# Kernel optimization log

Hardware: AMD Instinct MI355X
Metric: run time of the kernel (lower is better)

Reference implementation:

```python
import jax, jax.numpy as jnp
import numpy as np

B, NC, CN, K, DN = 2, 256, 256, 16, 64
G, HM, HS, HMOD, MOD_OUT = 8, 128, 128, 64, 5


def setup_inputs() -> dict:
    rng = np.random.default_rng(0)
    # per-neuron top-K neighbors within cell, excluding self, sorted (matches torch buffer build)
    scores = rng.random((NC, CN, CN)).astype(np.float32)
    ii = np.arange(CN)
    scores[:, ii, ii] = -np.inf
    conn = np.argpartition(-scores, K, axis=-1)[..., :K]
    conn = np.sort(conn, axis=-1).astype(np.int32)  # [NC, CN, K]

    key = jax.random.key(0)
    ks = jax.random.split(key, 12)
    n = lambda k, s, sc=1.0: jax.random.normal(k, s, jnp.float32) * sc
    return {
        'h': n(ks[0], (B, NC, CN, DN), 0.01),
        'w_conn': n(ks[1], (B, NC, CN, K), 0.1),
        'cell_context': n(ks[2], (B, NC, DN), 0.1),
        'neuron_id': n(ks[3], (NC, CN, DN), 0.02),
        'msg_w1': n(ks[4], (G, HM, 3 * DN), 0.05), 'msg_b1': jnp.zeros((G, HM)),
        'msg_w2': n(ks[5], (G, DN, HM), 0.005), 'msg_b2': jnp.zeros((G, DN)),
        'state_w1': n(ks[6], (G, HS, 3 * DN), 0.05), 'state_b1': jnp.zeros((G, HS)),
        'state_w2': n(ks[7], (G, DN, HS), 0.005), 'state_b2': jnp.zeros((G, DN)),
        'mod_w1': n(ks[8], (NC, 2 * DN, HMOD), 0.05), 'mod_b1': jnp.zeros((NC, HMOD)),
        'mod_w2': n(ks[9], (NC, HMOD, MOD_OUT), 0.0005), 'mod_b2': jnp.zeros((NC, MOD_OUT)),
        'conn_idx': jnp.asarray(conn),
        'cell_to_group': (jnp.arange(NC) % G).astype(jnp.int32),
    }


def reference(h, w_conn, cell_context, neuron_id,
              msg_w1, msg_b1, msg_w2, msg_b2,
              state_w1, state_b1, state_w2, state_b2,
              mod_w1, mod_b1, mod_w2, mod_b2,
              conn_idx, cell_to_group):
    nc = h.shape[1]
    cell_ix = jnp.arange(nc)[:, None, None]
    # gather K-neighbor states per neuron: [B, NC, CN, K, DN]
    nb = jax.vmap(lambda hb: hb[cell_ix, conn_idx])(h)
    # connection-weighted aggregation
    agg = jnp.einsum('bnck,bnckd->bncd', w_conn, nb)

    g = cell_to_group  # [NC]
    # grouped message MLP (2-layer), per-cell weights gathered from group table
    mfeat = jnp.concatenate([h, agg, jnp.broadcast_to(neuron_id[None], h.shape)], axis=-1)
    mh = jax.nn.gelu(jnp.einsum('bncf,nhf->bnch', mfeat, msg_w1[g]) + msg_b1[g][None, :, None, :])
    msg = jnp.einsum('bnch,ndh->bncd', mh, msg_w2[g]) + msg_b2[g][None, :, None, :]

    # grouped state MLP, residual update on h
    ctx = jnp.broadcast_to(cell_context[:, :, None, :], h.shape)
    sfeat = jnp.concatenate([h, msg, ctx], axis=-1)
    sh = jax.nn.gelu(jnp.einsum('bncf,nhf->bnch', sfeat, state_w1[g]) + state_b1[g][None, :, None, :])
    h_new = h + jnp.einsum('bnch,ndh->bncd', sh, state_w2[g]) + state_b2[g][None, :, None, :]

    # per-cell modulation MLP on pooled stats (h_mean || msg_mean)
    pooled = jnp.concatenate([h_new.mean(axis=2), msg.mean(axis=2)], axis=-1)  # [B, NC, 2DN]
    ph = jax.nn.gelu(jnp.einsum('bnf,nfh->bnh', pooled, mod_w1) + mod_b1[None])
    mod = jnp.einsum('bnh,nho->bno', ph, mod_w2) + mod_b2[None]
    return h_new, msg, mod
```

## Files before the change

### kernel.cpp

```cpp
#include <hip/hip_runtime.h>

#define B_   2
#define NC_  256
#define CN_  256
#define K_   16
#define DN_  64
#define G_   8
#define HM_  128
#define F3_  192

typedef unsigned short u16;
typedef short v8s __attribute__((ext_vector_type(8)));
typedef float v4f __attribute__((ext_vector_type(4)));

#define SMEM_BYTES 63616


__device__ __forceinline__ u16 f2b(float f) {
    unsigned v; __builtin_memcpy(&v, &f, 4);
    v = v + 0x7fffu + ((v >> 16) & 1u);
    return (u16)(v >> 16);
}
__device__ __forceinline__ v8s cvt8(const float* p) {
    float4 a = *(const float4*)p, b = *(const float4*)(p + 4);
    v8s r;
    r[0] = (short)f2b(a.x); r[1] = (short)f2b(a.y); r[2] = (short)f2b(a.z); r[3] = (short)f2b(a.w);
    r[4] = (short)f2b(b.x); r[5] = (short)f2b(b.y); r[6] = (short)f2b(b.z); r[7] = (short)f2b(b.w);
    return r;
}
__device__ __forceinline__ float gelu_t(float x) {
    float u = x * x;
    float t = 1.5957691216057308f * x * __builtin_fmaf(0.044715f, u, 1.0f);
    float e = __expf(-t);
    return x * __builtin_amdgcn_rcpf(1.0f + e);
}

__global__ __launch_bounds__(256) void cvt_w(
    const float* __restrict__ mw1, const float* __restrict__ mw2,
    const float* __restrict__ sw1, const float* __restrict__ sw2,
    u16* __restrict__ dst)
{
    int e = (blockIdx.x * 256 + threadIdx.x) * 4;
    const float* s; int off;
    if      (e < 196608) { s = mw1; off = e; }
    else if (e < 262144) { s = mw2; off = e - 196608; }
    else if (e < 458752) { s = sw1; off = e - 262144; }
    else                 { s = sw2; off = e - 458752; }
    float4 v = *(const float4*)(s + off);
    ushort4 o4;
    o4.x = f2b(v.x); o4.y = f2b(v.y); o4.z = f2b(v.z); o4.w = f2b(v.w);
    *(ushort4*)(dst + e) = o4;
}

__global__ __launch_bounds__(256, 2) void mg_main(
    const float* __restrict__ h,    const float* __restrict__ wconn,
    const float* __restrict__ ctx,  const float* __restrict__ nid,
    const u16* __restrict__ mw1b,   const float* __restrict__ mb1,
    const u16* __restrict__ mw2b,   const float* __restrict__ mb2,
    const u16* __restrict__ sw1b,   const float* __restrict__ sb1,
    const u16* __restrict__ sw2b,   const float* __restrict__ sb2,
    const int* __restrict__ conn,   const int* __restrict__ c2g,
    float* __restrict__ outf,       float* __restrict__ partial)
{
    const int bx   = blockIdx.x;
    const int bnc  = bx & 511;
    const int half = bx >> 9;
    const int r0   = half * 128;
    const int n    = bnc & 255;
    const int tid  = threadIdx.x;
    const int wave = tid >> 6;
    const int lane = tid & 63;
    const int q    = lane >> 4;
    const int ln   = lane & 15;
    const int g    = c2g[n];

    extern __shared__ char smem[];
    u16*   hbf  = (u16*)(smem);
    u16*   mh   = (u16*)(smem);
    u16*   am   = (u16*)(smem + 36864);
    u16*   ctxl = (u16*)(smem + 55296);
    float* hsum = (float*)(smem + 55424);
    float* msum = (float*)(smem + 59520);

    const size_t hbase = (size_t)bnc * (CN_ * DN_);
    const size_t nbase = (size_t)n   * (CN_ * DN_);
    float* oH = outf + (size_t)bnc * 16384;
    float* oM = outf + (size_t)8388608 + (size_t)bnc * 16384;

    if (tid < 64) ctxl[tid] = f2b(ctx[(size_t)bnc * DN_ + tid]);
    {
        const float* hrow = h + hbase + (size_t)tid * DN_;
        u16* drow = hbf + tid * 72;
#pragma unroll
        for (int i = 0; i < 8; ++i)
            *(v8s*)(drow + i * 8) = cvt8(hrow + i * 8);
    }
    __syncthreads();

    const int cbase = wave * 32;

    {
        const int kl = lane & 15;
        const int* cp       = conn + n * 4096 + (size_t)(r0 + cbase) * 16;
        const unsigned* wp  = (const unsigned*)(wconn + (size_t)bnc * 4096 + (size_t)(r0 + cbase) * 16);
        int ivv      = cp[kl];
        unsigned wvv = wp[kl];
        for (int c = 0; c < 32; ++c) {
            int ivn = 0; unsigned wvn = 0u;
            if (c < 31) { ivn = cp[(c + 1) * 16 + kl]; wvn = wp[(c + 1) * 16 + kl]; }
            float acc = 0.0f;
#pragma unroll
            for (int k = 0; k < 16; ++k) {
                int iv = __builtin_amdgcn_readlane(ivv, k);
                int wu = __builtin_amdgcn_readlane((int)wvv, k);
                unsigned hu = (unsigned)hbf[iv * 72 + lane] << 16;
                acc = __builtin_fmaf(__uint_as_float((unsigned)wu), __uint_as_float(hu), acc);
            }
            am[(cbase + c) * 72 + lane] = f2b(acc);
            ivv = ivn; wvv = wvn;
        }
    }

    v8s hfr[2][2], gfr[2][2], nfr[2][2];
#pragma unroll
    for (int mi = 0; mi < 2; ++mi) {
        int c = cbase + mi * 16 + ln;
        hfr[mi][0] = *(const v8s*)(hbf + (r0 + c) * 72 +  0 + q * 8);
        hfr[mi][1] = *(const v8s*)(hbf + (r0 + c) * 72 + 32 + q * 8);
        gfr[mi][0] = *(const v8s*)(am  + c * 72 +  0 + q * 8);
        gfr[mi][1] = *(const v8s*)(am  + c * 72 + 32 + q * 8);
        nfr[mi][0] = cvt8(nid + nbase + (size_t)(r0 + c) * 64 +  0 + q * 8);
        nfr[mi][1] = cvt8(nid + nbase + (size_t)(r0 + c) * 64 + 32 + q * 8);
    }
    __syncthreads();

    {
        v8s afr[6] = {hfr[0][0], hfr[0][1], gfr[0][0], gfr[0][1], nfr[0][0], nfr[0][1]};
        v8s afr1[6] = {hfr[1][0], hfr[1][1], gfr[1][0], gfr[1][1], nfr[1][0], nfr[1][1]};
        float b1v[8];
#pragma unroll
        for (int nt = 0; nt < 8; ++nt) b1v[nt] = mb1[g * HM_ + nt * 16 + ln];
        const u16* w1g = mw1b + (size_t)g * HM_ * F3_;
#pragma unroll
        for (int nt = 0; nt < 8; ++nt) {
            v4f acc0 = {0,0,0,0}, acc1 = {0,0,0,0};
#pragma unroll
            for (int ks = 0; ks < 6; ++ks) {
                v8s bf = *(const v8s*)(w1g + (nt * 16 + ln) * F3_ + ks * 32 + q * 8);
                acc0 = __builtin_amdgcn_mfma_f32_16x16x32_bf16(afr[ks],  bf, acc0, 0, 0, 0);
                acc1 = __builtin_amdgcn_mfma_f32_16x16x32_bf16(afr1[ks], bf, acc1, 0, 0, 0);
            }
            int c0 = cbase + q * 4, c1 = cbase + 16 + q * 4;
#pragma unroll
            for (int r = 0; r < 4; ++r) {
                mh[(c0 + r) * 136 + nt * 16 + ln] = f2b(gelu_t(acc0[r] + b1v[nt]));
                mh[(c1 + r) * 136 + nt * 16 + ln] = f2b(gelu_t(acc1[r] + b1v[nt]));
            }
        }
    }

    {
        v8s afr[2][4];
#pragma unroll
        for (int mi = 0; mi < 2; ++mi) {
            int c = cbase + mi * 16 + ln;
#pragma unroll
            for (int ks = 0; ks < 4; ++ks)
                afr[mi][ks] = *(const v8s*)(mh + c * 136 + ks * 32 + q * 8);
        }
        const u16* w2g = mw2b + (size_t)g * DN_ * HM_;
        float mpart[4];
#pragma unroll
        for (int nt = 0; nt < 4; ++nt) {
            float bb = mb2[g * DN_ + nt * 16 + ln];
            v4f acc[2] = {{0,0,0,0},{0,0,0,0}};
#pragma unroll
            for (int ks = 0; ks < 4; ++ks) {
                v8s bf = *(const v8s*)(w2g + (nt * 16 + ln) * HM_ + ks * 32 + q * 8);
#pragma unroll
                for (int mi = 0; mi < 2; ++mi)
                    acc[mi] = __builtin_amdgcn_mfma_f32_16x16x32_bf16(afr[mi][ks], bf, acc[mi], 0, 0, 0);
            }
            float ms = 0.0f;
            int d = nt * 16 + ln;
#pragma unroll
            for (int mi = 0; mi < 2; ++mi) {
                int c = cbase + mi * 16 + q * 4;
#pragma unroll
                for (int r = 0; r < 4; ++r) {
                    float mv = acc[mi][r] + bb;
                    am[(c + r) * 72 + d] = f2b(mv);
                    oM[(size_t)(r0 + c + r) * 64 + d] = mv;
                    ms += mv;
                }
            }
            mpart[nt] = ms;
        }
#pragma unroll
        for (int nt = 0; nt < 4; ++nt)
            msum[(wave * 4 + q) * 64 + nt * 16 + ln] = mpart[nt];
    }

    {
        v8s cfr0 = *(const v8s*)(ctxl +  0 + q * 8);
        v8s cfr1 = *(const v8s*)(ctxl + 32 + q * 8);
        v8s afr[2][4];
#pragma unroll
        for (int mi = 0; mi < 2; ++mi) {
            int c = cbase + mi * 16 + ln;
            afr[mi][0] = hfr[mi][0];
            afr[mi][1] = hfr[mi][1];
            afr[mi][2] = *(const v8s*)(am + c * 72 +  0 + q * 8);
            afr[mi][3] = *(const v8s*)(am + c * 72 + 32 + q * 8);
        }
        float b1v[8];
#pragma unroll
        for (int nt = 0; nt < 8; ++nt) b1v[nt] = sb1[g * HM_ + nt * 16 + ln];
        const u16* w1g = sw1b + (size_t)g * HM_ * F3_;
#pragma unroll
        for (int nt = 0; nt < 8; ++nt) {
            v4f acc[2] = {{0,0,0,0},{0,0,0,0}};
#pragma unroll
            for (int ks = 0; ks < 4; ++ks) {
                v8s bf = *(const v8s*)(w1g + (nt * 16 + ln) * F3_ + ks * 32 + q * 8);
#pragma unroll
                for (int mi = 0; mi < 2; ++mi)
                    acc[mi] = __builtin_amdgcn_mfma_f32_16x16x32_bf16(afr[mi][ks], bf, acc[mi], 0, 0, 0);
            }
#pragma unroll
            for (int ks = 4; ks < 6; ++ks) {
                v8s bf = *(const v8s*)(w1g + (nt * 16 + ln) * F3_ + ks * 32 + q * 8);
                v8s aa = (ks == 4) ? cfr0 : cfr1;
#pragma unroll
                for (int mi = 0; mi < 2; ++mi)
                    acc[mi] = __builtin_amdgcn_mfma_f32_16x16x32_bf16(aa, bf, acc[mi], 0, 0, 0);
            }
#pragma unroll
            for (int mi = 0; mi < 2; ++mi) {
                int c = cbase + mi * 16 + q * 4;
#pragma unroll
                for (int r = 0; r < 4; ++r)
                    mh[(c + r) * 136 + nt * 16 + ln] = f2b(gelu_t(acc[mi][r] + b1v[nt]));
            }
        }
    }

    {
        v8s afr[2][4];
#pragma unroll
        for (int mi = 0; mi < 2; ++mi) {
            int c = cbase + mi * 16 + ln;
#pragma unroll
            for (int ks = 0; ks < 4; ++ks)
                afr[mi][ks] = *(const v8s*)(mh + c * 136 + ks * 32 + q * 8);
        }
        const u16* w2g = sw2b + (size_t)g * DN_ * HM_;
        float hpart[4];
#pragma unroll
        for (int nt = 0; nt < 4; ++nt) {
            float bb = sb2[g * DN_ + nt * 16 + ln];
            v4f acc[2] = {{0,0,0,0},{0,0,0,0}};
#pragma unroll
            for (int ks = 0; ks < 4; ++ks) {
                v8s bf = *(const v8s*)(w2g + (nt * 16 + ln) * HM_ + ks * 32 + q * 8);
#pragma unroll
                for (int mi = 0; mi < 2; ++mi)
                    acc[mi] = __builtin_amdgcn_mfma_f32_16x16x32_bf16(afr[mi][ks], bf, acc[mi], 0, 0, 0);
            }
            float hs = 0.0f;
            int d = nt * 16 + ln;
#pragma unroll
            for (int mi = 0; mi < 2; ++mi) {
                int c = cbase + mi * 16 + q * 4;
#pragma unroll
                for (int r = 0; r < 4; ++r) {
                    float hv = h[hbase + (size_t)(r0 + c + r) * 64 + d];
                    float hn = hv + acc[mi][r] + bb;
                    oH[(size_t)(r0 + c + r) * 64 + d] = hn;
                    hs += hn;
                }
            }
            hpart[nt] = hs;
        }
#pragma unroll
        for (int nt = 0; nt < 4; ++nt)
            hsum[(wave * 4 + q) * 64 + nt * 16 + ln] = hpart[nt];
    }
    __syncthreads();

    if (tid < 128) {
        int col = tid & 63;
        const float* src = (tid < 64) ? hsum : msum;
        float s = 0.0f;
#pragma unroll
        for (int i = 0; i < 16; ++i) s += src[i * 64 + col];
        partial[(size_t)(bnc * 2 + half) * 128 + (tid < 64 ? col : 64 + col)] = s * (1.0f / 256.0f);
    }
}

__global__ __launch_bounds__(256) void mg_mod(
    const float* __restrict__ w1, const float* __restrict__ b1,
    const float* __restrict__ w2, const float* __restrict__ b2,
    const float* __restrict__ partial, float* __restrict__ outf)
{
    __shared__ float pool[128];
    __shared__ float ph4[4][64];
    const int bnc = blockIdx.x, n = bnc & 255, t = threadIdx.x;
    if (t < 128)
        pool[t] = partial[(size_t)(bnc * 2) * 128 + t] + partial[(size_t)(bnc * 2 + 1) * 128 + t];
    __syncthreads();
    {
        const int col = t & 63, fh = t >> 6;
        const float* w1p = w1 + ((size_t)n * 128 + fh * 32) * 64 + col;
        float acc = 0.0f;
#pragma unroll
        for (int i = 0; i < 32; ++i)
            acc = __builtin_fmaf(pool[fh * 32 + i], w1p[(size_t)i * 64], acc);
        ph4[fh][col] = acc;
    }
    __syncthreads();
    if (t < 64) {
        float a  = ph4[0][t] + ph4[1][t] + ph4[2][t] + ph4[3][t] + b1[n * 64 + t];
        float ph = gelu_t(a);
        float part5[5];
#pragma unroll
        for (int o = 0; o < 5; ++o) part5[o] = ph * w2[((size_t)n * 64 + t) * 5 + o];
#pragma unroll
        for (int off = 32; off > 0; off >>= 1)
#pragma unroll
            for (int o = 0; o < 5; ++o) part5[o] += __shfl_down(part5[o], off);
        if (t == 0) {
#pragma unroll
            for (int o = 0; o < 5; ++o)
                outf[(size_t)16777216 + bnc * 5 + o] = part5[o] + b2[n * 5 + o];
        }
    }
}

extern "C" void kernel_launch(void* const* d_in, const int* in_sizes, int n_in,
                              void* d_out, int out_size, void* d_ws, size_t ws_size,
                              hipStream_t stream) {
    const float* h     = (const float*)d_in[0];
    const float* wconn = (const float*)d_in[1];
    const float* ctx   = (const float*)d_in[2];
    const float* nid   = (const float*)d_in[3];
    const float* mw1   = (const float*)d_in[4];
    const float* mb1   = (const float*)d_in[5];
    const float* mw2   = (const float*)d_in[6];
    const float* mb2   = (const float*)d_in[7];
    const float* sw1   = (const float*)d_in[8];
    const float* sb1   = (const float*)d_in[9];
    const float* sw2   = (const float*)d_in[10];
    const float* sb2   = (const float*)d_in[11];
    const float* dw1   = (const float*)d_in[12];
    const float* db1   = (const float*)d_in[13];
    const float* dw2   = (const float*)d_in[14];
    const float* db2   = (const float*)d_in[15];
    const int* conn    = (const int*)d_in[16];
    const int* c2g     = (const int*)d_in[17];
    float* outf   = (float*)d_out;
    u16*   wb     = (u16*)d_ws;
    float* partial = (float*)((char*)d_ws + 1048576);

    hipFuncSetAttribute(reinterpret_cast<const void*>(&mg_main),
                        hipFuncAttributeMaxDynamicSharedMemorySize, SMEM_BYTES);

    cvt_w<<<512, 256, 0, stream>>>(mw1, mw2, sw1, sw2, wb);
    mg_main<<<1024, 256, SMEM_BYTES, stream>>>(h, wconn, ctx, nid,
                                               wb,           mb1,
                                               wb + 196608,  mb2,
                                               wb + 262144,  sb1,
                                               wb + 458752,  sb2,
                                               conn, c2g, outf, partial);
    mg_mod<<<512, 256, 0, stream>>>(dw1, db1, dw2, db2, partial, outf);
}
```

Before: 239.1 us.

## Shrink shared memory to fit three blocks per CU and streamline gather

Shared memory per block shrinks by narrowing the h row pitch to 68, dropping the separate ctx and sum buffers, and keeping the partial sums in the padding columns of the aggregation buffer. Launch bounds move to three blocks per CU. The neighbor gather now loads indices and weights through scalar, wave-uniform addresses with double buffering, and uses two accumulators instead of readlane. The h and neuron_id MFMA fragments are reloaded from global memory and the column sums are reduced with shuffles. These changes aim for higher occupancy, paid for by extra global reloads, more register pressure, and possible LDS bank conflicts from the new pitch.

```diff
diff --git a/kernel.cpp b/kernel.cpp
--- a/kernel.cpp
+++ b/kernel.cpp
@@ -11,9 +11,10 @@
 
 typedef unsigned short u16;
 typedef short v8s __attribute__((ext_vector_type(8)));
+typedef short v4s __attribute__((ext_vector_type(4)));
 typedef float v4f __attribute__((ext_vector_type(4)));
 
-#define SMEM_BYTES 63616
+#define SMEM_BYTES 53248
 
 
 __device__ __forceinline__ u16 f2b(float f) {
@@ -52,7 +53,20 @@
     *(ushort4*)(dst + e) = o4;
 }
 
-__global__ __launch_bounds__(256, 2) void mg_main(
+#define GATHER_ROW(cc, ivv, wvv)                                              \
+    {                                                                         \
+        float acc0 = 0.0f, acc1 = 0.0f;                                       \
+        _Pragma("unroll")                                                     \
+        for (int k = 0; k < 16; k += 2) {                                     \
+            unsigned h0 = (unsigned)hbf[ivv[k] * 68 + lane];                  \
+            unsigned h1 = (unsigned)hbf[ivv[k + 1] * 68 + lane];              \
+            acc0 = __builtin_fmaf(wvv[k],     __uint_as_float(h0 << 16), acc0); \
+            acc1 = __builtin_fmaf(wvv[k + 1], __uint_as_float(h1 << 16), acc1); \
+        }                                                                     \
+        am[(cbase + (cc)) * 72 + lane] = f2b(acc0 + acc1);                    \
+    }
+
+__global__ __launch_bounds__(256, 3) void mg_main(
     const float* __restrict__ h,    const float* __restrict__ wconn,
     const float* __restrict__ ctx,  const float* __restrict__ nid,
     const u16* __restrict__ mw1b,   const float* __restrict__ mb1,
@@ -75,68 +89,74 @@
     const int g    = c2g[n];
 
     extern __shared__ char smem[];
-    u16*   hbf  = (u16*)(smem);
-    u16*   mh   = (u16*)(smem);
-    u16*   am   = (u16*)(smem + 36864);
-    u16*   ctxl = (u16*)(smem + 55296);
-    float* hsum = (float*)(smem + 55424);
-    float* msum = (float*)(smem + 59520);
+    u16* hbf = (u16*)(smem);
+    u16* mh  = (u16*)(smem);
+    u16* am  = (u16*)(smem + 34816);
 
     const size_t hbase = (size_t)bnc * (CN_ * DN_);
     const size_t nbase = (size_t)n   * (CN_ * DN_);
     float* oH = outf + (size_t)bnc * 16384;
     float* oM = outf + (size_t)8388608 + (size_t)bnc * 16384;
 
-    if (tid < 64) ctxl[tid] = f2b(ctx[(size_t)bnc * DN_ + tid]);
     {
         const float* hrow = h + hbase + (size_t)tid * DN_;
-        u16* drow = hbf + tid * 72;
-#pragma unroll
-        for (int i = 0; i < 8; ++i)
-            *(v8s*)(drow + i * 8) = cvt8(hrow + i * 8);
+        u16* drow = hbf + tid * 68;
+#pragma unroll
+        for (int i = 0; i < 8; ++i) {
+            v8s v = cvt8(hrow + i * 8);
+            *(v4s*)(drow + i * 8)     = __builtin_shufflevector(v, v, 0, 1, 2, 3);
+            *(v4s*)(drow + i * 8 + 4) = __builtin_shufflevector(v, v, 4, 5, 6, 7);
+        }
     }
     __syncthreads();
 
     const int cbase = wave * 32;
 
     {
-        const int kl = lane & 15;
-        const int* cp       = conn + n * 4096 + (size_t)(r0 + cbase) * 16;
-        const unsigned* wp  = (const unsigned*)(wconn + (size_t)bnc * 4096 + (size_t)(r0 + cbase) * 16);
-        int ivv      = cp[kl];
-        unsigned wvv = wp[kl];
-        for (int c = 0; c < 32; ++c) {
-            int ivn = 0; unsigned wvn = 0u;
-            if (c < 31) { ivn = cp[(c + 1) * 16 + kl]; wvn = wp[(c + 1) * 16 + kl]; }
-            float acc = 0.0f;
+        const int wrow0 = __builtin_amdgcn_readfirstlane(r0 + cbase);
+        const int*   __restrict__ cp = conn  + n * 4096 + wrow0 * 16;
+        const float* __restrict__ wp = wconn + (size_t)bnc * 4096 + (size_t)wrow0 * 16;
+        int ivA[16], ivB[16]; float wvA[16], wvB[16];
+#pragma unroll
+        for (int k = 0; k < 16; ++k) { ivA[k] = cp[k]; wvA[k] = wp[k]; }
+        for (int c = 0; c < 32; c += 2) {
 #pragma unroll
             for (int k = 0; k < 16; ++k) {
-                int iv = __builtin_amdgcn_readlane(ivv, k);
-                int wu = __builtin_amdgcn_readlane((int)wvv, k);
-                unsigned hu = (unsigned)hbf[iv * 72 + lane] << 16;
-                acc = __builtin_fmaf(__uint_as_float((unsigned)wu), __uint_as_float(hu), acc);
-            }
-            am[(cbase + c) * 72 + lane] = f2b(acc);
-            ivv = ivn; wvv = wvn;
-        }
-    }
-
-    v8s hfr[2][2], gfr[2][2], nfr[2][2];
-#pragma unroll
-    for (int mi = 0; mi < 2; ++mi) {
-        int c = cbase + mi * 16 + ln;
-        hfr[mi][0] = *(const v8s*)(hbf + (r0 + c) * 72 +  0 + q * 8);
-        hfr[mi][1] = *(const v8s*)(hbf + (r0 + c) * 72 + 32 + q * 8);
-        gfr[mi][0] = *(const v8s*)(am  + c * 72 +  0 + q * 8);
-        gfr[mi][1] = *(const v8s*)(am  + c * 72 + 32 + q * 8);
-        nfr[mi][0] = cvt8(nid + nbase + (size_t)(r0 + c) * 64 +  0 + q * 8);
-        nfr[mi][1] = cvt8(nid + nbase + (size_t)(r0 + c) * 64 + 32 + q * 8);
+                ivB[k] = cp[(c + 1) * 16 + k]; wvB[k] = wp[(c + 1) * 16 + k];
+            }
+            GATHER_ROW(c, ivA, wvA)
+            if (c + 2 < 32) {
+#pragma unroll
+                for (int k = 0; k < 16; ++k) {
+                    ivA[k] = cp[(c + 2) * 16 + k]; wvA[k] = wp[(c + 2) * 16 + k];
+                }
+            }
+            GATHER_ROW(c + 1, ivB, wvB)
+        }
     }
     __syncthreads();
 
-    {
-        v8s afr[6] = {hfr[0][0], hfr[0][1], gfr[0][0], gfr[0][1], nfr[0][0], nfr[0][1]};
-        v8s afr1[6] = {hfr[1][0], hfr[1][1], gfr[1][0], gfr[1][1], nfr[1][0], nfr[1][1]};
+    v8s hfr0[2], hfr1[2], gfr0[2], gfr1[2], nfr0[2], nfr1[2];
+    {
+        int c0 = r0 + cbase + ln, c1 = r0 + cbase + 16 + ln;
+        hfr0[0] = cvt8(h + hbase + (size_t)c0 * 64 +  0 + q * 8);
+        hfr0[1] = cvt8(h + hbase + (size_t)c0 * 64 + 32 + q * 8);
+        hfr1[0] = cvt8(h + hbase + (size_t)c1 * 64 +  0 + q * 8);
+        hfr1[1] = cvt8(h + hbase + (size_t)c1 * 64 + 32 + q * 8);
+        nfr0[0] = cvt8(nid + nbase + (size_t)c0 * 64 +  0 + q * 8);
+        nfr0[1] = cvt8(nid + nbase + (size_t)c0 * 64 + 32 + q * 8);
+        nfr1[0] = cvt8(nid + nbase + (size_t)c1 * 64 +  0 + q * 8);
+        nfr1[1] = cvt8(nid + nbase + (size_t)c1 * 64 + 32 + q * 8);
+        int lc0 = cbase + ln, lc1 = cbase + 16 + ln;
+        gfr0[0] = *(const v8s*)(am + lc0 * 72 +  0 + q * 8);
+        gfr0[1] = *(const v8s*)(am + lc0 * 72 + 32 + q * 8);
+        gfr1[0] = *(const v8s*)(am + lc1 * 72 +  0 + q * 8);
+        gfr1[1] = *(const v8s*)(am + lc1 * 72 + 32 + q * 8);
+    }
+
+    {
+        v8s afr0[6] = {hfr0[0], hfr0[1], gfr0[0], gfr0[1], nfr0[0], nfr0[1]};
+        v8s afr1[6] = {hfr1[0], hfr1[1], gfr1[0], gfr1[1], nfr1[0], nfr1[1]};
         float b1v[8];
 #pragma unroll
         for (int nt = 0; nt < 8; ++nt) b1v[nt] = mb1[g * HM_ + nt * 16 + ln];
@@ -147,7 +167,7 @@
 #pragma unroll
             for (int ks = 0; ks < 6; ++ks) {
                 v8s bf = *(const v8s*)(w1g + (nt * 16 + ln) * F3_ + ks * 32 + q * 8);
-                acc0 = __builtin_amdgcn_mfma_f32_16x16x32_bf16(afr[ks],  bf, acc0, 0, 0, 0);
+                acc0 = __builtin_amdgcn_mfma_f32_16x16x32_bf16(afr0[ks], bf, acc0, 0, 0, 0);
                 acc1 = __builtin_amdgcn_mfma_f32_16x16x32_bf16(afr1[ks], bf, acc1, 0, 0, 0);
             }
             int c0 = cbase + q * 4, c1 = cbase + 16 + q * 4;
@@ -197,19 +217,26 @@
             mpart[nt] = ms;
         }
 #pragma unroll
-        for (int nt = 0; nt < 4; ++nt)
-            msum[(wave * 4 + q) * 64 + nt * 16 + ln] = mpart[nt];
-    }
-
-    {
-        v8s cfr0 = *(const v8s*)(ctxl +  0 + q * 8);
-        v8s cfr1 = *(const v8s*)(ctxl + 32 + q * 8);
+        for (int nt = 0; nt < 4; ++nt) {
+            float v = mpart[nt];
+            v += __shfl_xor(v, 16);
+            v += __shfl_xor(v, 32);
+            if (q == 0) {
+                int i = 256 + wave * 64 + nt * 16 + ln;
+                *((float*)(am + (i >> 2) * 72 + 64) + (i & 3)) = v;
+            }
+        }
+    }
+
+    {
+        v8s cfr0 = cvt8(ctx + (size_t)bnc * DN_ +  0 + q * 8);
+        v8s cfr1 = cvt8(ctx + (size_t)bnc * DN_ + 32 + q * 8);
         v8s afr[2][4];
 #pragma unroll
         for (int mi = 0; mi < 2; ++mi) {
             int c = cbase + mi * 16 + ln;
-            afr[mi][0] = hfr[mi][0];
-            afr[mi][1] = hfr[mi][1];
+            afr[mi][0] = (mi == 0) ? hfr0[0] : hfr1[0];
+            afr[mi][1] = (mi == 0) ? hfr0[1] : hfr1[1];
             afr[mi][2] = *(const v8s*)(am + c * 72 +  0 + q * 8);
             afr[mi][3] = *(const v8s*)(am + c * 72 + 32 + q * 8);
         }
@@ -283,17 +310,27 @@
             hpart[nt] = hs;
         }
 #pragma unroll
-        for (int nt = 0; nt < 4; ++nt)
-            hsum[(wave * 4 + q) * 64 + nt * 16 + ln] = hpart[nt];
+        for (int nt = 0; nt < 4; ++nt) {
+            float v = hpart[nt];
+            v += __shfl_xor(v, 16);
+            v += __shfl_xor(v, 32);
+            if (q == 0) {
+                int i = wave * 64 + nt * 16 + ln;
+                *((float*)(am + (i >> 2) * 72 + 64) + (i & 3)) = v;
+            }
+        }
     }
     __syncthreads();
 
     if (tid < 128) {
-        int col = tid & 63;
-        const float* src = (tid < 64) ? hsum : msum;
+        int col  = tid & 63;
+        int base = (tid < 64) ? 0 : 256;
         float s = 0.0f;
 #pragma unroll
-        for (int i = 0; i < 16; ++i) s += src[i * 64 + col];
+        for (int w = 0; w < 4; ++w) {
+            int i = base + w * 64 + col;
+            s += *((const float*)(am + (i >> 2) * 72 + 64) + (i & 3));
+        }
         partial[(size_t)(bnc * 2 + half) * 128 + (tid < 64 ? col : 64 + col)] = s * (1.0f / 256.0f);
     }
 }
```

Measured after the change: 287.9 us. 1.2x slower.

## Split neighbor gather into separate kernel and shrink MLP blocks to single wave

Applied to the files above, without the earlier changes.

The neighbor aggregation moves out of the main kernel into its own gather kernel, which reads fp32 h straight from global memory and writes agg into the msg output buffer as scratch. The MLP kernel then runs as 4096 one-wave blocks of 32 rows each, using small static LDS with padded strides and no block barriers. Per-block pooled sums are reduced with cross-lane shuffles into 8 partials per cell, which the modulation kernel now sums. The aim is more parallelism and less LDS pressure, at the cost of an extra launch and a global round trip for agg.

```diff
diff --git a/kernel.cpp b/kernel.cpp
--- a/kernel.cpp
+++ b/kernel.cpp
@@ -1,6 +1,5 @@
 #include <hip/hip_runtime.h>
 
-#define B_   2
 #define NC_  256
 #define CN_  256
 #define K_   16
@@ -12,8 +11,6 @@
 typedef unsigned short u16;
 typedef short v8s __attribute__((ext_vector_type(8)));
 typedef float v4f __attribute__((ext_vector_type(4)));
-
-#define SMEM_BYTES 63616
 
 
 __device__ __forceinline__ u16 f2b(float f) {
@@ -52,90 +49,84 @@
     *(ushort4*)(dst + e) = o4;
 }
 
-__global__ __launch_bounds__(256, 2) void mg_main(
-    const float* __restrict__ h,    const float* __restrict__ wconn,
-    const float* __restrict__ ctx,  const float* __restrict__ nid,
+__global__ __launch_bounds__(256) void gth(
+    const float* __restrict__ h, const float* __restrict__ wconn,
+    const int* __restrict__ conn, float* __restrict__ outf)
+{
+    const int p     = blockIdx.x;
+    const int bnc   = (p & 7) * 64 + (p >> 6);
+    const int chunk = (p >> 3) & 7;
+    const int wave  = threadIdx.x >> 6, lane = threadIdx.x & 63;
+    const int r0    = chunk * 32 + wave * 8;
+    const int n     = bnc & 255;
+    const size_t hb = (size_t)bnc * 16384;
+    const float* __restrict__ hp = h + hb;
+    float* aggo = outf + (size_t)8388608 + hb;
+    const int*   __restrict__ cp = conn  + n * 4096 + r0 * 16;
+    const float* __restrict__ wp = wconn + (size_t)bnc * 4096 + (size_t)r0 * 16;
+    int   ivA = cp[lane],      ivB = cp[64 + lane];
+    float wvA = wp[lane],      wvB = wp[64 + lane];
+#pragma unroll
+    for (int i = 0; i < 8; ++i) {
+        int   iv = (i < 4) ? ivA : ivB;
+        float wv = (i < 4) ? wvA : wvB;
+        float a0 = 0.0f, a1 = 0.0f;
+#pragma unroll
+        for (int k = 0; k < 16; k += 2) {
+            const int l0 = (i & 3) * 16 + k;
+            int   i0 = __builtin_amdgcn_readlane(iv, l0);
+            int   i1 = __builtin_amdgcn_readlane(iv, l0 + 1);
+            float w0 = __int_as_float(__builtin_amdgcn_readlane(__float_as_int(wv), l0));
+            float w1 = __int_as_float(__builtin_amdgcn_readlane(__float_as_int(wv), l0 + 1));
+            a0 = __builtin_fmaf(w0, hp[i0 * 64 + lane], a0);
+            a1 = __builtin_fmaf(w1, hp[i1 * 64 + lane], a1);
+        }
+        aggo[(size_t)(r0 + i) * 64 + lane] = a0 + a1;
+    }
+}
+
+__global__ __launch_bounds__(64, 3) void mg_main(
+    const float* __restrict__ h,    const float* __restrict__ ctx,
+    const float* __restrict__ nid,
     const u16* __restrict__ mw1b,   const float* __restrict__ mb1,
     const u16* __restrict__ mw2b,   const float* __restrict__ mb2,
     const u16* __restrict__ sw1b,   const float* __restrict__ sb1,
     const u16* __restrict__ sw2b,   const float* __restrict__ sb2,
-    const int* __restrict__ conn,   const int* __restrict__ c2g,
+    const int* __restrict__ c2g,
     float* __restrict__ outf,       float* __restrict__ partial)
 {
-    const int bx   = blockIdx.x;
-    const int bnc  = bx & 511;
-    const int half = bx >> 9;
-    const int r0   = half * 128;
-    const int n    = bnc & 255;
-    const int tid  = threadIdx.x;
-    const int wave = tid >> 6;
-    const int lane = tid & 63;
-    const int q    = lane >> 4;
-    const int ln   = lane & 15;
-    const int g    = c2g[n];
-
-    extern __shared__ char smem[];
-    u16*   hbf  = (u16*)(smem);
-    u16*   mh   = (u16*)(smem);
-    u16*   am   = (u16*)(smem + 36864);
-    u16*   ctxl = (u16*)(smem + 55296);
-    float* hsum = (float*)(smem + 55424);
-    float* msum = (float*)(smem + 59520);
-
-    const size_t hbase = (size_t)bnc * (CN_ * DN_);
-    const size_t nbase = (size_t)n   * (CN_ * DN_);
-    float* oH = outf + (size_t)bnc * 16384;
-    float* oM = outf + (size_t)8388608 + (size_t)bnc * 16384;
-
-    if (tid < 64) ctxl[tid] = f2b(ctx[(size_t)bnc * DN_ + tid]);
-    {
-        const float* hrow = h + hbase + (size_t)tid * DN_;
-        u16* drow = hbf + tid * 72;
-#pragma unroll
-        for (int i = 0; i < 8; ++i)
-            *(v8s*)(drow + i * 8) = cvt8(hrow + i * 8);
-    }
-    __syncthreads();
-
-    const int cbase = wave * 32;
-
-    {
-        const int kl = lane & 15;
-        const int* cp       = conn + n * 4096 + (size_t)(r0 + cbase) * 16;
-        const unsigned* wp  = (const unsigned*)(wconn + (size_t)bnc * 4096 + (size_t)(r0 + cbase) * 16);
-        int ivv      = cp[kl];
-        unsigned wvv = wp[kl];
-        for (int c = 0; c < 32; ++c) {
-            int ivn = 0; unsigned wvn = 0u;
-            if (c < 31) { ivn = cp[(c + 1) * 16 + kl]; wvn = wp[(c + 1) * 16 + kl]; }
-            float acc = 0.0f;
-#pragma unroll
-            for (int k = 0; k < 16; ++k) {
-                int iv = __builtin_amdgcn_readlane(ivv, k);
-                int wu = __builtin_amdgcn_readlane((int)wvv, k);
-                unsigned hu = (unsigned)hbf[iv * 72 + lane] << 16;
-                acc = __builtin_fmaf(__uint_as_float((unsigned)wu), __uint_as_float(hu), acc);
-            }
-            am[(cbase + c) * 72 + lane] = f2b(acc);
-            ivv = ivn; wvv = wvn;
-        }
-    }
+    const int p     = blockIdx.x;
+    const int bnc   = (p & 7) * 64 + (p >> 6);
+    const int chunk = (p >> 3) & 7;
+    const int r0    = chunk * 32;
+    const int n     = bnc & 255;
+    const int g     = c2g[n];
+    const int lane  = threadIdx.x;
+    const int q     = lane >> 4, ln = lane & 15;
+
+    __shared__ u16 mh[32 * 138];
+    __shared__ u16 am[32 * 74];
+
+    const size_t hbase = (size_t)bnc * 16384;
+    const size_t nbase = (size_t)n   * 16384;
+    float* oH = outf + hbase;
+    float* oM = outf + (size_t)8388608 + hbase;
+    const size_t pbase = (size_t)(bnc * 8 + chunk) * 128;
 
     v8s hfr[2][2], gfr[2][2], nfr[2][2];
 #pragma unroll
     for (int mi = 0; mi < 2; ++mi) {
-        int c = cbase + mi * 16 + ln;
-        hfr[mi][0] = *(const v8s*)(hbf + (r0 + c) * 72 +  0 + q * 8);
-        hfr[mi][1] = *(const v8s*)(hbf + (r0 + c) * 72 + 32 + q * 8);
-        gfr[mi][0] = *(const v8s*)(am  + c * 72 +  0 + q * 8);
-        gfr[mi][1] = *(const v8s*)(am  + c * 72 + 32 + q * 8);
-        nfr[mi][0] = cvt8(nid + nbase + (size_t)(r0 + c) * 64 +  0 + q * 8);
-        nfr[mi][1] = cvt8(nid + nbase + (size_t)(r0 + c) * 64 + 32 + q * 8);
-    }
-    __syncthreads();
-
-    {
-        v8s afr[6] = {hfr[0][0], hfr[0][1], gfr[0][0], gfr[0][1], nfr[0][0], nfr[0][1]};
+        int c = r0 + mi * 16 + ln;
+        hfr[mi][0] = cvt8(h   + hbase + (size_t)c * 64 +  0 + q * 8);
+        hfr[mi][1] = cvt8(h   + hbase + (size_t)c * 64 + 32 + q * 8);
+        gfr[mi][0] = cvt8(oM  + (size_t)c * 64 +  0 + q * 8);
+        gfr[mi][1] = cvt8(oM  + (size_t)c * 64 + 32 + q * 8);
+        nfr[mi][0] = cvt8(nid + nbase + (size_t)c * 64 +  0 + q * 8);
+        nfr[mi][1] = cvt8(nid + nbase + (size_t)c * 64 + 32 + q * 8);
+    }
+
+    {
+        v8s afr0[6] = {hfr[0][0], hfr[0][1], gfr[0][0], gfr[0][1], nfr[0][0], nfr[0][1]};
         v8s afr1[6] = {hfr[1][0], hfr[1][1], gfr[1][0], gfr[1][1], nfr[1][0], nfr[1][1]};
         float b1v[8];
 #pragma unroll
@@ -147,14 +138,14 @@
 #pragma unroll
             for (int ks = 0; ks < 6; ++ks) {
                 v8s bf = *(const v8s*)(w1g + (nt * 16 + ln) * F3_ + ks * 32 + q * 8);
-                acc0 = __builtin_amdgcn_mfma_f32_16x16x32_bf16(afr[ks],  bf, acc0, 0, 0, 0);
+                acc0 = __builtin_amdgcn_mfma_f32_16x16x32_bf16(afr0[ks], bf, acc0, 0, 0, 0);
                 acc1 = __builtin_amdgcn_mfma_f32_16x16x32_bf16(afr1[ks], bf, acc1, 0, 0, 0);
             }
-            int c0 = cbase + q * 4, c1 = cbase + 16 + q * 4;
+            int c0 = q * 4, c1 = 16 + q * 4;
 #pragma unroll
             for (int r = 0; r < 4; ++r) {
-                mh[(c0 + r) * 136 + nt * 16 + ln] = f2b(gelu_t(acc0[r] + b1v[nt]));
-                mh[(c1 + r) * 136 + nt * 16 + ln] = f2b(gelu_t(acc1[r] + b1v[nt]));
+                mh[(c0 + r) * 138 + nt * 16 + ln] = f2b(gelu_t(acc0[r] + b1v[nt]));
+                mh[(c1 + r) * 138 + nt * 16 + ln] = f2b(gelu_t(acc1[r] + b1v[nt]));
             }
         }
     }
@@ -163,10 +154,10 @@
         v8s afr[2][4];
 #pragma unroll
         for (int mi = 0; mi < 2; ++mi) {
-            int c = cbase + mi * 16 + ln;
+            int c = mi * 16 + ln;
 #pragma unroll
             for (int ks = 0; ks < 4; ++ks)
-                afr[mi][ks] = *(const v8s*)(mh + c * 136 + ks * 32 + q * 8);
+                afr[mi][ks] = *(const v8s*)(mh + c * 138 + ks * 32 + q * 8);
         }
         const u16* w2g = mw2b + (size_t)g * DN_ * HM_;
         float mpart[4];
@@ -185,11 +176,11 @@
             int d = nt * 16 + ln;
 #pragma unroll
             for (int mi = 0; mi < 2; ++mi) {
-                int c = cbase + mi * 16 + q * 4;
+                int c = mi * 16 + q * 4;
 #pragma unroll
                 for (int r = 0; r < 4; ++r) {
                     float mv = acc[mi][r] + bb;
-                    am[(c + r) * 72 + d] = f2b(mv);
+                    am[(c + r) * 74 + d] = f2b(mv);
                     oM[(size_t)(r0 + c + r) * 64 + d] = mv;
                     ms += mv;
                 }
@@ -197,21 +188,25 @@
             mpart[nt] = ms;
         }
 #pragma unroll
-        for (int nt = 0; nt < 4; ++nt)
-            msum[(wave * 4 + q) * 64 + nt * 16 + ln] = mpart[nt];
-    }
-
-    {
-        v8s cfr0 = *(const v8s*)(ctxl +  0 + q * 8);
-        v8s cfr1 = *(const v8s*)(ctxl + 32 + q * 8);
+        for (int nt = 0; nt < 4; ++nt) {
+            float v = mpart[nt];
+            v += __shfl_xor(v, 16);
+            v += __shfl_xor(v, 32);
+            if (q == 0) partial[pbase + 64 + nt * 16 + ln] = v * (1.0f / 256.0f);
+        }
+    }
+
+    {
+        v8s cfr0 = cvt8(ctx + (size_t)bnc * DN_ +  0 + q * 8);
+        v8s cfr1 = cvt8(ctx + (size_t)bnc * DN_ + 32 + q * 8);
         v8s afr[2][4];
 #pragma unroll
         for (int mi = 0; mi < 2; ++mi) {
-            int c = cbase + mi * 16 + ln;
+            int c = mi * 16 + ln;
             afr[mi][0] = hfr[mi][0];
             afr[mi][1] = hfr[mi][1];
-            afr[mi][2] = *(const v8s*)(am + c * 72 +  0 + q * 8);
-            afr[mi][3] = *(const v8s*)(am + c * 72 + 32 + q * 8);
+            afr[mi][2] = *(const v8s*)(am + c * 74 +  0 + q * 8);
+            afr[mi][3] = *(const v8s*)(am + c * 74 + 32 + q * 8);
         }
         float b1v[8];
 #pragma unroll
@@ -237,10 +232,10 @@
             }
 #pragma unroll
             for (int mi = 0; mi < 2; ++mi) {
-                int c = cbase + mi * 16 + q * 4;
+                int c = mi * 16 + q * 4;
 #pragma unroll
                 for (int r = 0; r < 4; ++r)
-                    mh[(c + r) * 136 + nt * 16 + ln] = f2b(gelu_t(acc[mi][r] + b1v[nt]));
+                    mh[(c + r) * 138 + nt * 16 + ln] = f2b(gelu_t(acc[mi][r] + b1v[nt]));
             }
         }
     }
@@ -249,10 +244,10 @@
         v8s afr[2][4];
 #pragma unroll
         for (int mi = 0; mi < 2; ++mi) {
-            int c = cbase + mi * 16 + ln;
+            int c = mi * 16 + ln;
 #pragma unroll
             for (int ks = 0; ks < 4; ++ks)
-                afr[mi][ks] = *(const v8s*)(mh + c * 136 + ks * 32 + q * 8);
+                afr[mi][ks] = *(const v8s*)(mh + c * 138 + ks * 32 + q * 8);
         }
         const u16* w2g = sw2b + (size_t)g * DN_ * HM_;
         float hpart[4];
@@ -271,7 +266,7 @@
             int d = nt * 16 + ln;
 #pragma unroll
             for (int mi = 0; mi < 2; ++mi) {
-                int c = cbase + mi * 16 + q * 4;
+                int c = mi * 16 + q * 4;
 #pragma unroll
                 for (int r = 0; r < 4; ++r) {
                     float hv = h[hbase + (size_t)(r0 + c + r) * 64 + d];
@@ -283,18 +278,12 @@
             hpart[nt] = hs;
         }
 #pragma unroll
-        for (int nt = 0; nt < 4; ++nt)
-            hsum[(wave * 4 + q) * 64 + nt * 16 + ln] = hpart[nt];
-    }
-    __syncthreads();
-
-    if (tid < 128) {
-        int col = tid & 63;
-        const float* src = (tid < 64) ? hsum : msum;
-        float s = 0.0f;
-#pragma unroll
-        for (int i = 0; i < 16; ++i) s += src[i * 64 + col];
-        partial[(size_t)(bnc * 2 + half) * 128 + (tid < 64 ? col : 64 + col)] = s * (1.0f / 256.0f);
+        for (int nt = 0; nt < 4; ++nt) {
+            float v = hpart[nt];
+            v += __shfl_xor(v, 16);
+            v += __shfl_xor(v, 32);
+            if (q == 0) partial[pbase + nt * 16 + ln] = v * (1.0f / 256.0f);
+        }
     }
 }
 
@@ -306,8 +295,13 @@
     __shared__ float pool[128];
     __shared__ float ph4[4][64];
     const int bnc = blockIdx.x, n = bnc & 255, t = threadIdx.x;
-    if (t < 128)
-        pool[t] = partial[(size_t)(bnc * 2) * 128 + t] + partial[(size_t)(bnc * 2 + 1) * 128 + t];
+    if (t < 128) {
+        const float* pp = partial + (size_t)bnc * 1024 + t;
+        float s = 0.0f;
+#pragma unroll
+        for (int j = 0; j < 8; ++j) s += pp[j * 128];
+        pool[t] = s;
+    }
     __syncthreads();
     {
         const int col = t & 63, fh = t >> 6;
@@ -358,19 +352,17 @@
     const float* db2   = (const float*)d_in[15];
     const int* conn    = (const int*)d_in[16];
     const int* c2g     = (const int*)d_in[17];
-    float* outf   = (float*)d_out;
-    u16*   wb     = (u16*)d_ws;
+    float* outf    = (float*)d_out;
+    u16*   wb      = (u16*)d_ws;
     float* partial = (float*)((char*)d_ws + 1048576);
 
-    hipFuncSetAttribute(reinterpret_cast<const void*>(&mg_main),
-                        hipFuncAttributeMaxDynamicSharedMemorySize, SMEM_BYTES);
-
     cvt_w<<<512, 256, 0, stream>>>(mw1, mw2, sw1, sw2, wb);
-    mg_main<<<1024, 256, SMEM_BYTES, stream>>>(h, wconn, ctx, nid,
-                                               wb,           mb1,
-                                               wb + 196608,  mb2,
-                                               wb + 262144,  sb1,
-                                               wb + 458752,  sb2,
-                                               conn, c2g, outf, partial);
+    gth<<<4096, 256, 0, stream>>>(h, wconn, conn, outf);
+    mg_main<<<4096, 64, 0, stream>>>(h, ctx, nid,
+                                     wb,           mb1,
+                                     wb + 196608,  mb2,
+                                     wb + 262144,  sb1,
+                                     wb + 458752,  sb2,
+                                     c2g, outf, partial);
     mg_mod<<<512, 256, 0, stream>>>(dw1, db1, dw2, db2, partial, outf);
 }
```

New measurement: 259.8 us. +8.7%, slower.
